# Kernel optimization log

Hardware: AMD Instinct MI355X
Metric: run time of the kernel (lower is better)

## Reference

```python
import jax, jax.numpy as jnp
import numpy as np


def setup_inputs() -> dict:
    key = jax.random.key(0)
    k_x, k0, k1, k2, kb = jax.random.split(key, 5)
    D, C, KH, KW = 256, 128, 3, 3
    R1, R2 = 8, 4
    x = jax.random.normal(k_x, (32, C, 64, 64), dtype=jnp.float32)
    # TT cores (leading/trailing rank-1 dims squeezed), init U(-0.77, 0.77) as in the torch module
    core0 = jax.random.uniform(k0, (D, C, R1), dtype=jnp.float32, minval=-0.77, maxval=0.77)
    core1 = jax.random.uniform(k1, (D, R1, KH, R2), dtype=jnp.float32, minval=-0.77, maxval=0.77)
    core2 = jax.random.uniform(k2, (D, R2, KW), dtype=jnp.float32, minval=-0.77, maxval=0.77)
    bias = jax.random.uniform(kb, (1,), dtype=jnp.float32, minval=-0.1, maxval=0.1)
    return {"x": x, "core0": core0, "core1": core1, "core2": core2,
            "bias": bias, "stride": 1, "pad": 1}


def reference(x, core0, core1, core2, bias, stride, pad):
    # Reconstruct the full conv kernel from the TT cores: [D, C, kH, kW]
    kernel = jnp.einsum('dcr,drks,dsj->dckj', core0, core1, core2)
    # Same math as pad + unfold + einsum('nchwkj,dckj->ndhw'): a standard cross-correlation conv
    out = jax.lax.conv_general_dilated(
        x, kernel,
        window_strides=(stride, stride),
        padding=[(pad, pad), (pad, pad)],
        dimension_numbers=('NCHW', 'OIHW', 'NCHW'))
    # scalar bias broadcast over all output channels (bias.view(1,-1,1,1) with 1 element)
    return out + bias.reshape(1, -1, 1, 1)
```

## Files before the change

kernel.cpp:

```cpp
#include <hip/hip_runtime.h>

typedef __bf16 bf16x8 __attribute__((ext_vector_type(8)));
typedef float f32x4 __attribute__((ext_vector_type(4)));

__device__ __forceinline__ unsigned short f2bf(float f) {
    union { float f; unsigned int u; } v; v.f = f;
    unsigned int u = v.u;
    unsigned int r = (u + 0x7fffu + ((u >> 16) & 1u)) >> 16;
    return (unsigned short)r;
}

__global__ void build_w_kernel(const float* __restrict__ core0,
                               const float* __restrict__ core1,
                               const float* __restrict__ core2,
                               unsigned short* __restrict__ wb) {
    __shared__ float s1[96];
    __shared__ float s2[12];
    const int d = blockIdx.x;
    const int c = threadIdx.x;
    if (c < 96) s1[c] = core1[d * 96 + c];
    if (c >= 96 && c < 108) s2[c - 96] = core2[d * 12 + (c - 96)];
    __syncthreads();
    float t0[8];
#pragma unroll
    for (int r = 0; r < 8; ++r) t0[r] = core0[(d * 128 + c) * 8 + r];
#pragma unroll
    for (int kh = 0; kh < 3; ++kh) {
        float v[4] = {0.f, 0.f, 0.f, 0.f};
#pragma unroll
        for (int r = 0; r < 8; ++r)
#pragma unroll
            for (int s = 0; s < 4; ++s)
                v[s] += t0[r] * s1[(r * 3 + kh) * 4 + s];
#pragma unroll
        for (int kw = 0; kw < 3; ++kw) {
            float val = 0.f;
#pragma unroll
            for (int s = 0; s < 4; ++s) val += v[s] * s2[s * 3 + kw];
            const int kidx = (kh * 3 + kw) * 128 + c;
            wb[(kidx >> 3) * 2048 + d * 8 + (kidx & 7)] = f2bf(val);
        }
    }
}

#define LC 136

__global__ __launch_bounds__(256, 3) void conv_mfma_kernel(
    const float* __restrict__ x, const unsigned short* __restrict__ wb,
    const float* __restrict__ bias, float* __restrict__ out) {
    __shared__ __align__(16) unsigned short xl[3 * 66 * LC];

    const int tid  = threadIdx.x;
    const int lane = tid & 63;
    const int wv   = tid >> 6;
    const int l15  = lane & 15;
    const int quad = lane >> 4;
    const int bid  = blockIdx.x;
    const int n    = bid >> 6;
    const int h    = bid & 63;

    if (tid < 96) {
        const int row = tid >> 5;
        const int j   = tid & 31;
        const int col = (j >> 4) ? 65 : 0;
        const int c   = (j & 15) << 3;
        *(uint4*)(xl + (row * 66 + col) * LC + c) = make_uint4(0u, 0u, 0u, 0u);
    }

#pragma unroll 2
    for (int i = 0; i < 6; ++i) {
        const int it  = tid + (i << 8);
        const int w4  = it & 15;
        const int cg  = (it >> 4) & 31;
        const int row = it >> 9;
        const int rimg = h + row - 1;
        float4 p0 = make_float4(0.f, 0.f, 0.f, 0.f), p1 = p0, p2 = p0, p3 = p0;
        const int c = cg << 2;
        const int w = w4 << 2;
        if (rimg >= 0 && rimg < 64) {
            const float4* gp = (const float4*)(x + (((n * 128 + c) * 64 + rimg) * 64 + w));
            p0 = gp[0];
            p1 = gp[1024];
            p2 = gp[2048];
            p3 = gp[3072];
        }
        unsigned short* base = xl + (row * 66 + w + 1) * LC + c;
        *(ushort4*)(base)          = make_ushort4(f2bf(p0.x), f2bf(p1.x), f2bf(p2.x), f2bf(p3.x));
        *(ushort4*)(base + LC)     = make_ushort4(f2bf(p0.y), f2bf(p1.y), f2bf(p2.y), f2bf(p3.y));
        *(ushort4*)(base + 2 * LC) = make_ushort4(f2bf(p0.z), f2bf(p1.z), f2bf(p2.z), f2bf(p3.z));
        *(ushort4*)(base + 3 * LC) = make_ushort4(f2bf(p0.w), f2bf(p1.w), f2bf(p2.w), f2bf(p3.w));
    }
    __syncthreads();

    f32x4 acc[4][4];
#pragma unroll
    for (int a0 = 0; a0 < 4; ++a0)
#pragma unroll
        for (int b0 = 0; b0 < 4; ++b0) acc[a0][b0] = (f32x4){0.f, 0.f, 0.f, 0.f};

    const int dwave = wv << 6;
    const bf16x8* wgv = (const bf16x8*)wb;
    const int abase = quad * 256 + dwave + l15;

    bf16x8 an[4];
#pragma unroll
    for (int dt = 0; dt < 4; ++dt) an[dt] = wgv[abase + dt * 16];

    const unsigned short* bb = xl + l15 * LC + quad * 8;

#pragma unroll
    for (int tap = 0; tap < 9; ++tap) {
        const int kh = tap / 3;
        const int kw = tap - kh * 3;
#pragma unroll
        for (int c4 = 0; c4 < 4; ++c4) {
            const int ch = tap * 4 + c4;
            bf16x8 ac[4];
#pragma unroll
            for (int dt = 0; dt < 4; ++dt) ac[dt] = an[dt];
            if (ch + 1 < 36) {
                const bf16x8* g2 = wgv + (ch + 1) * 1024 + abase;
#pragma unroll
                for (int dt = 0; dt < 4; ++dt) an[dt] = g2[dt * 16];
            }
            const int c0 = c4 << 5;
            bf16x8 bfr[4];
            const unsigned short* bp = bb + (kh * 66 + kw) * LC + c0;
#pragma unroll
            for (int pt = 0; pt < 4; ++pt) bfr[pt] = *(const bf16x8*)(bp + pt * 16 * LC);
#pragma unroll
            for (int dt = 0; dt < 4; ++dt)
#pragma unroll
                for (int pt = 0; pt < 4; ++pt)
                    acc[dt][pt] = __builtin_amdgcn_mfma_f32_16x16x32_bf16(
                        ac[dt], bfr[pt], acc[dt][pt], 0, 0, 0);
        }
    }

    const float bv = bias[0];
#pragma unroll
    for (int dt = 0; dt < 4; ++dt) {
#pragma unroll
        for (int pt = 0; pt < 4; ++pt) {
#pragma unroll
            for (int r = 0; r < 4; ++r) {
                const int d = dwave + dt * 16 + quad * 4 + r;
                const int w = pt * 16 + l15;
                out[((n * 256 + d) * 64 + h) * 64 + w] = acc[dt][pt][r] + bv;
            }
        }
    }
}

extern "C" void kernel_launch(void* const* d_in, const int* in_sizes, int n_in,
                              void* d_out, int out_size, void* d_ws, size_t ws_size,
                              hipStream_t stream) {
    const float* x     = (const float*)d_in[0];
    const float* core0 = (const float*)d_in[1];
    const float* core1 = (const float*)d_in[2];
    const float* core2 = (const float*)d_in[3];
    const float* bias  = (const float*)d_in[4];
    unsigned short* wb = (unsigned short*)d_ws;

    build_w_kernel<<<256, 128, 0, stream>>>(core0, core1, core2, wb);
    conv_mfma_kernel<<<2048, 256, 0, stream>>>(x, wb, bias, (float*)d_out);
}
```

Baseline: 248.8 us.

## Process four output rows per block with a ring-buffered input tile and prefetch

Each block now computes four output rows, in two passes of two rows each, instead of one. The input is held in a four-slot LDS ring of rows, so halo rows are shared and global reads of x drop from 3x to 1.5x. Each A-fragment of weights feeds two rows of MFMAs, and the next pass's rows are prefetched into registers during the first pass. The trade-off is twice the accumulators, a lower occupancy target (launch bounds 2), and a grid of only 512 blocks, which may leave CUs underfilled.

After: 347.0 us. +39.5%, slower.

```diff
diff --git a/kernel.cpp b/kernel.cpp
--- a/kernel.cpp
+++ b/kernel.cpp
@@ -43,12 +43,107 @@
     }
 }
 
-#define LC 136
-
-__global__ __launch_bounds__(256, 3) void conv_mfma_kernel(
+#define LC   136
+#define SLOT (66 * LC)
+
+__device__ __forceinline__ void load_row_unit(const float* __restrict__ x,
+                                              int n, int rimg, int tid, int u,
+                                              float4 p[4]) {
+    const int it = tid + (u << 8);
+    const int w4 = it & 15;
+    const int cg = it >> 4;
+    p[0] = p[1] = p[2] = p[3] = make_float4(0.f, 0.f, 0.f, 0.f);
+    if (rimg >= 0 && rimg < 64) {
+        const float4* gp = (const float4*)(x + (((n * 128 + (cg << 2)) * 64 + rimg) << 6) + (w4 << 2));
+        p[0] = gp[0];
+        p[1] = gp[1024];
+        p[2] = gp[2048];
+        p[3] = gp[3072];
+    }
+}
+
+__device__ __forceinline__ void write_row_unit(unsigned short* xl, int slot,
+                                               int tid, int u, const float4 p[4]) {
+    const int it = tid + (u << 8);
+    const int w4 = it & 15;
+    const int cg = it >> 4;
+    unsigned short* base = xl + slot * SLOT + ((w4 << 2) + 1) * LC + (cg << 2);
+    *(ushort4*)(base)          = make_ushort4(f2bf(p[0].x), f2bf(p[1].x), f2bf(p[2].x), f2bf(p[3].x));
+    *(ushort4*)(base + LC)     = make_ushort4(f2bf(p[0].y), f2bf(p[1].y), f2bf(p[2].y), f2bf(p[3].y));
+    *(ushort4*)(base + 2 * LC) = make_ushort4(f2bf(p[0].z), f2bf(p[1].z), f2bf(p[2].z), f2bf(p[3].z));
+    *(ushort4*)(base + 3 * LC) = make_ushort4(f2bf(p[0].w), f2bf(p[1].w), f2bf(p[2].w), f2bf(p[3].w));
+}
+
+__device__ __forceinline__ void kloop_pass(const bf16x8* __restrict__ wgv,
+                                           const unsigned short* __restrict__ xl,
+                                           int hb,
+                                           int abase, int l15, int quad,
+                                           f32x4 acc[4][8]) {
+    bf16x8 an[4];
+#pragma unroll
+    for (int dt = 0; dt < 4; ++dt) an[dt] = wgv[abase + dt * 16];
+#pragma unroll
+    for (int tap = 0; tap < 9; ++tap) {
+        const int kh = tap / 3;
+        const int kw = tap - kh * 3;
+        const int sA = (hb + kh) & 3;
+        const int sB = (hb + kh + 1) & 3;
+        const unsigned short* baseA = xl + sA * SLOT + (l15 + kw) * LC + quad * 8;
+        const unsigned short* baseB = xl + sB * SLOT + (l15 + kw) * LC + quad * 8;
+#pragma unroll
+        for (int c4 = 0; c4 < 4; ++c4) {
+            const int ch = tap * 4 + c4;
+            bf16x8 ac[4];
+#pragma unroll
+            for (int dt = 0; dt < 4; ++dt) ac[dt] = an[dt];
+            if (ch + 1 < 36) {
+                const bf16x8* g2 = wgv + (ch + 1) * 1024 + abase;
+#pragma unroll
+                for (int dt = 0; dt < 4; ++dt) an[dt] = g2[dt * 16];
+            }
+            const int c0 = c4 << 5;
+            bf16x8 b0[4];
+#pragma unroll
+            for (int pt = 0; pt < 4; ++pt) b0[pt] = *(const bf16x8*)(baseA + pt * 16 * LC + c0);
+#pragma unroll
+            for (int dt = 0; dt < 4; ++dt)
+#pragma unroll
+                for (int pt = 0; pt < 4; ++pt)
+                    acc[dt][pt] = __builtin_amdgcn_mfma_f32_16x16x32_bf16(
+                        ac[dt], b0[pt], acc[dt][pt], 0, 0, 0);
+            bf16x8 b1[4];
+#pragma unroll
+            for (int pt = 0; pt < 4; ++pt) b1[pt] = *(const bf16x8*)(baseB + pt * 16 * LC + c0);
+#pragma unroll
+            for (int dt = 0; dt < 4; ++dt)
+#pragma unroll
+                for (int pt = 0; pt < 4; ++pt)
+                    acc[dt][4 + pt] = __builtin_amdgcn_mfma_f32_16x16x32_bf16(
+                        ac[dt], b1[pt], acc[dt][4 + pt], 0, 0, 0);
+        }
+    }
+}
+
+__device__ __forceinline__ void epilogue(float* __restrict__ out, const f32x4 acc[4][8],
+                                         int n, int hA, int dwave, int quad, int l15,
+                                         float bv) {
+#pragma unroll
+    for (int dt = 0; dt < 4; ++dt)
+#pragma unroll
+        for (int pt = 0; pt < 8; ++pt) {
+            const int d  = dwave + dt * 16 + quad * 4;
+            const int hh = hA + (pt >> 2);
+            const int w  = (pt & 3) * 16 + l15;
+            float* op = out + ((n * 256 + d) * 64 + hh) * 64 + w;
+#pragma unroll
+            for (int r = 0; r < 4; ++r) op[r * 4096] = acc[dt][pt][r] + bv;
+        }
+}
+
+__global__ __launch_bounds__(256, 2) void conv_mfma_kernel(
     const float* __restrict__ x, const unsigned short* __restrict__ wb,
     const float* __restrict__ bias, float* __restrict__ out) {
-    __shared__ __align__(16) unsigned short xl[3 * 66 * LC];
+    __shared__ __align__(16) unsigned short xl[4 * SLOT];
 
     const int tid  = threadIdx.x;
     const int lane = tid & 63;
@@ -56,100 +151,66 @@
     const int l15  = lane & 15;
     const int quad = lane >> 4;
     const int bid  = blockIdx.x;
-    const int n    = bid >> 6;
-    const int h    = bid & 63;
-
-    if (tid < 96) {
-        const int row = tid >> 5;
-        const int j   = tid & 31;
-        const int col = (j >> 4) ? 65 : 0;
-        const int c   = (j & 15) << 3;
-        *(uint4*)(xl + (row * 66 + col) * LC + c) = make_uint4(0u, 0u, 0u, 0u);
-    }
-
-#pragma unroll 2
-    for (int i = 0; i < 6; ++i) {
-        const int it  = tid + (i << 8);
-        const int w4  = it & 15;
-        const int cg  = (it >> 4) & 31;
-        const int row = it >> 9;
-        const int rimg = h + row - 1;
-        float4 p0 = make_float4(0.f, 0.f, 0.f, 0.f), p1 = p0, p2 = p0, p3 = p0;
-        const int c = cg << 2;
-        const int w = w4 << 2;
-        if (rimg >= 0 && rimg < 64) {
-            const float4* gp = (const float4*)(x + (((n * 128 + c) * 64 + rimg) * 64 + w));
-            p0 = gp[0];
-            p1 = gp[1024];
-            p2 = gp[2048];
-            p3 = gp[3072];
-        }
-        unsigned short* base = xl + (row * 66 + w + 1) * LC + c;
-        *(ushort4*)(base)          = make_ushort4(f2bf(p0.x), f2bf(p1.x), f2bf(p2.x), f2bf(p3.x));
-        *(ushort4*)(base + LC)     = make_ushort4(f2bf(p0.y), f2bf(p1.y), f2bf(p2.y), f2bf(p3.y));
-        *(ushort4*)(base + 2 * LC) = make_ushort4(f2bf(p0.z), f2bf(p1.z), f2bf(p2.z), f2bf(p3.z));
-        *(ushort4*)(base + 3 * LC) = make_ushort4(f2bf(p0.w), f2bf(p1.w), f2bf(p2.w), f2bf(p3.w));
-    }
-    __syncthreads();
-
-    f32x4 acc[4][4];
+    const int n    = bid >> 4;
+    const int h0   = (bid & 15) << 2;
+
+    if (tid < 128) {
+        const int slot = tid >> 5;
+        const int j    = tid & 31;
+        const int col  = (j >> 4) ? 65 : 0;
+        const int c    = (j & 15) << 3;
+        *(uint4*)(xl + slot * SLOT + col * LC + c) = make_uint4(0u, 0u, 0u, 0u);
+    }
+
+#pragma unroll
+    for (int row = 0; row < 4; ++row) {
+        const int rimg = h0 - 1 + row;
+#pragma unroll
+        for (int u = 0; u < 2; ++u) {
+            float4 p[4];
+            load_row_unit(x, n, rimg, tid, u, p);
+            write_row_unit(xl, row, tid, u, p);
+        }
+    }
+    __syncthreads();
+
+    const bf16x8* wgv = (const bf16x8*)wb;
+    const int dwave = wv << 6;
+    const int abase = quad * 256 + dwave + l15;
+    const float bv = bias[0];
+
+    float4 pfA[2][4];
+    load_row_unit(x, n, h0 + 3, tid, 0, pfA[0]);
+    load_row_unit(x, n, h0 + 3, tid, 1, pfA[1]);
+
+    f32x4 acc[4][8];
 #pragma unroll
     for (int a0 = 0; a0 < 4; ++a0)
 #pragma unroll
-        for (int b0 = 0; b0 < 4; ++b0) acc[a0][b0] = (f32x4){0.f, 0.f, 0.f, 0.f};
-
-    const int dwave = wv << 6;
-    const bf16x8* wgv = (const bf16x8*)wb;
-    const int abase = quad * 256 + dwave + l15;
-
-    bf16x8 an[4];
-#pragma unroll
-    for (int dt = 0; dt < 4; ++dt) an[dt] = wgv[abase + dt * 16];
-
-    const unsigned short* bb = xl + l15 * LC + quad * 8;
-
-#pragma unroll
-    for (int tap = 0; tap < 9; ++tap) {
-        const int kh = tap / 3;
-        const int kw = tap - kh * 3;
-#pragma unroll
-        for (int c4 = 0; c4 < 4; ++c4) {
-            const int ch = tap * 4 + c4;
-            bf16x8 ac[4];
-#pragma unroll
-            for (int dt = 0; dt < 4; ++dt) ac[dt] = an[dt];
-            if (ch + 1 < 36) {
-                const bf16x8* g2 = wgv + (ch + 1) * 1024 + abase;
-#pragma unroll
-                for (int dt = 0; dt < 4; ++dt) an[dt] = g2[dt * 16];
-            }
-            const int c0 = c4 << 5;
-            bf16x8 bfr[4];
-            const unsigned short* bp = bb + (kh * 66 + kw) * LC + c0;
-#pragma unroll
-            for (int pt = 0; pt < 4; ++pt) bfr[pt] = *(const bf16x8*)(bp + pt * 16 * LC);
-#pragma unroll
-            for (int dt = 0; dt < 4; ++dt)
-#pragma unroll
-                for (int pt = 0; pt < 4; ++pt)
-                    acc[dt][pt] = __builtin_amdgcn_mfma_f32_16x16x32_bf16(
-                        ac[dt], bfr[pt], acc[dt][pt], 0, 0, 0);
-        }
-    }
-
-    const float bv = bias[0];
-#pragma unroll
-    for (int dt = 0; dt < 4; ++dt) {
-#pragma unroll
-        for (int pt = 0; pt < 4; ++pt) {
-#pragma unroll
-            for (int r = 0; r < 4; ++r) {
-                const int d = dwave + dt * 16 + quad * 4 + r;
-                const int w = pt * 16 + l15;
-                out[((n * 256 + d) * 64 + h) * 64 + w] = acc[dt][pt][r] + bv;
-            }
-        }
-    }
+        for (int b0 = 0; b0 < 8; ++b0) acc[a0][b0] = (f32x4){0.f, 0.f, 0.f, 0.f};
+
+    kloop_pass(wgv, xl, 0, abase, l15, quad, acc);
+
+    float4 pfB[2][4];
+    load_row_unit(x, n, h0 + 4, tid, 0, pfB[0]);
+    load_row_unit(x, n, h0 + 4, tid, 1, pfB[1]);
+
+    __syncthreads();
+    write_row_unit(xl, 0, tid, 0, pfA[0]);
+    write_row_unit(xl, 0, tid, 1, pfA[1]);
+    write_row_unit(xl, 1, tid, 0, pfB[0]);
+    write_row_unit(xl, 1, tid, 1, pfB[1]);
+    __syncthreads();
+
+    epilogue(out, acc, n, h0, dwave, quad, l15, bv);
+
+#pragma unroll
+    for (int a0 = 0; a0 < 4; ++a0)
+#pragma unroll
+        for (int b0 = 0; b0 < 8; ++b0) acc[a0][b0] = (f32x4){0.f, 0.f, 0.f, 0.f};
+
+    kloop_pass(wgv, xl, 2, abase, l15, quad, acc);
+    epilogue(out, acc, n, h0 + 2, dwave, quad, l15, bv);
 }
 
 extern "C" void kernel_launch(void* const* d_in, const int* in_sizes, int n_in,
@@ -163,5 +224,5 @@
     unsigned short* wb = (unsigned short*)d_ws;
 
     build_w_kernel<<<256, 128, 0, stream>>>(core0, core1, core2, wb);
-    conv_mfma_kernel<<<2048, 256, 0, stream>>>(x, wb, bias, (float*)d_out);
-}
+    conv_mfma_kernel<<<512, 256, 0, stream>>>(x, wb, bias, (float*)d_out);
+}
```
